# Kernel tuning notes

Hardware: AMD Instinct MI355X
Metric: run time of the kernel (lower is better)

Reference implementation:

```python
import jax, jax.numpy as jnp
import numpy as np

TEMPERATURE = 1.0
B, H, S, D = 2, 16, 2048, 128

def setup_inputs() -> dict:
    key = jax.random.key(0)
    kq, kk, kv = jax.random.split(key, 3)
    q = jax.random.normal(kq, (B, H, S, D), dtype=jnp.float32)
    k = jax.random.normal(kk, (B, H, S, D), dtype=jnp.float32)
    v = jax.random.normal(kv, (B, H, S, D), dtype=jnp.float32)
    alpha = jnp.float32(0.5)  # nn.Parameter(torch.tensor(0.5))
    return {"q": q, "k": k, "v": v, "alpha": alpha}

def reference(q, k, v, alpha):
    # scores: [B,H,S,S]
    scores = jnp.einsum('bhqd,bhkd->bhqk', q, k) / TEMPERATURE
    row_mean = jnp.mean(scores, axis=-1, keepdims=True)  # [B,H,S,1]
    adaptive = alpha * scores + (1.0 - alpha) * row_mean
    attn = jax.nn.softmax(adaptive, axis=-1)
    return jnp.einsum('bhqk,bhkd->bhqd', attn, v)
```

## Files before the change

### kernel.cpp

```cpp
#include <hip/hip_runtime.h>


#define S_LEN 2048
#define HD    128
#define BQ    64
#define BK    64
#define NW    2
#define NT    (S_LEN / BK)
#define KTILE_USH 8192
#define VTILE_USH 8192
#define VBASE_USH (32 * NT * KTILE_USH)

typedef __bf16    bf16x8 __attribute__((ext_vector_type(8)));
typedef __bf16    bf16x4 __attribute__((ext_vector_type(4)));
typedef _Float16  f16x8  __attribute__((ext_vector_type(8)));
typedef float     f32x4  __attribute__((ext_vector_type(4)));

__device__ __forceinline__ unsigned short f2bf(float x) {
  unsigned u = __builtin_bit_cast(unsigned, x);
  u = (u + 0x7FFFu + ((u >> 16) & 1u)) >> 16;
  return (unsigned short)u;
}
__device__ __forceinline__ unsigned short f2h(float x) {
  _Float16 h = (_Float16)x;
  return __builtin_bit_cast(unsigned short, h);
}
__device__ __forceinline__ float fast_exp2(float x) {
#if __has_builtin(__builtin_amdgcn_exp2f)
  return __builtin_amdgcn_exp2f(x);
#else
  return exp2f(x);
#endif
}

__global__ __launch_bounds__(256) void attn_prepass_kernel(
    const float* __restrict__ kg, const float* __restrict__ vg,
    unsigned short* __restrict__ ws) {
  __shared__ float T[64 * 130];
  const int blk  = blockIdx.x;
  const int head = blk >> 5;
  const int kt   = blk & 31;
  const int tid  = threadIdx.x;
  const size_t hoff = (size_t)head * S_LEN * HD;
  const float* kp = kg + hoff + (size_t)kt * BK * HD;
  const float* vp = vg + hoff + (size_t)kt * BK * HD;
  unsigned short* wsK = ws + (size_t)blk * KTILE_USH;
  unsigned short* wsV = ws + VBASE_USH + (size_t)blk * VTILE_USH;

#pragma unroll
  for (int it = 0; it < 4; ++it) {
    int idx = it * 256 + tid;
    int key = idx >> 4;
    int ch  = idx & 15;
    const float* src = kp + key * HD + ch * 8;
    float4 a = *(const float4*)src;
    float4 b = *(const float4*)(src + 4);
    float xs[8] = {a.x, a.y, a.z, a.w, b.x, b.y, b.z, b.w};
    union { unsigned short s[8]; uint4 v; } hi;
#pragma unroll
    for (int j = 0; j < 8; ++j) hi.s[j] = f2h(xs[j]);
    int slot = (ch & 8) | ((ch & 7) ^ (key & 7));
    *(uint4*)&wsK[key * 128 + slot * 8] = hi.v;
  }

#pragma unroll
  for (int it = 0; it < 16; ++it) {
    int idx = it * 256 + tid;
    int key = idx >> 6;
    int c2  = idx & 63;
    float2 a = *(const float2*)(vp + (size_t)key * HD + c2 * 2);
    *(float2*)&T[key * 130 + c2 * 2] = a;
  }
  __syncthreads();

#pragma unroll
  for (int r = 0; r < 4; ++r) {
    int idx = r * 256 + tid;
    int dim = idx >> 3;
    int ch  = idx & 7;
    union { unsigned short s[8]; uint4 v; } gg;
#pragma unroll
    for (int j = 0; j < 8; ++j) gg.s[j] = f2bf(T[(ch * 8 + j) * 130 + dim]);
    int gidx = ((dim >> 4) * 2 + (ch >> 2)) * 64 + (ch & 3) * 16 + (dim & 15);
    *(uint4*)&wsV[gidx * 8] = gg.v;
  }
}

__device__ __forceinline__ void stage_k(const unsigned short* __restrict__ wt,
                                        unsigned short* dst, int tid, int w) {
#pragma unroll
  for (int r = 0; r < 8; ++r) {
    const unsigned int* gp = (const unsigned int*)(wt + (size_t)(r * 128 + tid) * 8);
    unsigned short* lp = dst + (size_t)(r * 128 + w * 64) * 8;
    __builtin_amdgcn_global_load_lds(
        (const __attribute__((address_space(1))) unsigned int*)gp,
        (__attribute__((address_space(3))) unsigned int*)lp, 16, 0, 0);
  }
}

__global__ __launch_bounds__(128, 2) void adaptive_attn_kernel(
    const float* __restrict__ qg, const unsigned short* __restrict__ ws,
    const float* __restrict__ alphap, float* __restrict__ out) {
  __shared__ unsigned short sBuf[2][KTILE_USH];
  __shared__ unsigned short sP[NW][2][1024];

  const int b    = blockIdx.x;
  const int head = (b & 7) * 4 + ((b >> 3) & 3);
  const int qt   = b >> 5;

  const int tid  = threadIdx.x;
  const int w    = tid >> 6;
  const int lane = tid & 63;
  const int g    = lane >> 4;
  const int qi   = lane & 15;

  const float lscale = alphap[0] * 1.44269504088896f;

  f16x8 qf[2][4];
#pragma unroll
  for (int h = 0; h < 2; ++h) {
    const int qrow = qt * BQ + w * 32 + h * 16 + qi;
    const float* qp = qg + (size_t)head * S_LEN * HD + (size_t)qrow * HD;
#pragma unroll
    for (int c = 0; c < 4; ++c) {
      float4 a  = *(const float4*)(qp + c * 32 + g * 8);
      float4 bb = *(const float4*)(qp + c * 32 + g * 8 + 4);
      float xs[8] = {a.x, a.y, a.z, a.w, bb.x, bb.y, bb.z, bb.w};
      union { f16x8 v; _Float16 s[8]; } hh;
#pragma unroll
      for (int j = 0; j < 8; ++j) hh.s[j] = (_Float16)(xs[j] * lscale);
      qf[h][c] = hh.v;
    }
  }

  f32x4 o[2][8];
#pragma unroll
  for (int h = 0; h < 2; ++h)
#pragma unroll
    for (int dt = 0; dt < 8; ++dt) o[h][dt] = (f32x4){0.f, 0.f, 0.f, 0.f};
  float lrun[2] = {0.f, 0.f};

  const unsigned short* wsKh = ws + (size_t)head * NT * KTILE_USH;
  const unsigned short* wsVh = ws + VBASE_USH + (size_t)head * NT * VTILE_USH;

  stage_k(wsKh, &sBuf[0][0], tid, w);
  __syncthreads();

  for (int kt = 0; kt < NT; ++kt) {
    const unsigned short* sK = &sBuf[kt & 1][0];

    const unsigned short* vb = wsVh + (size_t)kt * VTILE_USH;
    bf16x8 vf[8][2];
#pragma unroll
    for (int dt = 0; dt < 8; ++dt)
#pragma unroll
      for (int c = 0; c < 2; ++c)
        vf[dt][c] = *(const bf16x8*)&vb[((dt * 2 + c) * 64 + lane) * 8];

    if (kt + 1 < NT)
      stage_k(wsKh + (size_t)(kt + 1) * KTILE_USH, &sBuf[(kt + 1) & 1][0], tid, w);

    f32x4 st[2][4];
    __builtin_amdgcn_s_setprio(1);
#pragma unroll
    for (int mt = 0; mt < 4; ++mt) {
      f32x4 a0 = (f32x4){0.f, 0.f, 0.f, 0.f};
      f32x4 a1 = (f32x4){0.f, 0.f, 0.f, 0.f};
#pragma unroll
      for (int c = 0; c < 4; ++c) {
        int ch   = c * 4 + g;
        int slot = (ch & 8) | ((ch & 7) ^ (qi & 7));
        f16x8 ah = *(const f16x8*)&sK[(mt * 16 + qi) * 128 + slot * 8];
        a0 = __builtin_amdgcn_mfma_f32_16x16x32_f16(ah, qf[0][c], a0, 0, 0, 0);
        a1 = __builtin_amdgcn_mfma_f32_16x16x32_f16(ah, qf[1][c], a1, 0, 0, 0);
      }
      st[0][mt] = a0; st[1][mt] = a1;
    }
    __builtin_amdgcn_s_setprio(0);

#pragma unroll
    for (int h = 0; h < 2; ++h) {
      unsigned short* sPh = &sP[w][h][0];
#pragma unroll
      for (int mt = 0; mt < 4; ++mt) {
        float p0 = fast_exp2(st[h][mt][0]);
        float p1 = fast_exp2(st[h][mt][1]);
        float p2 = fast_exp2(st[h][mt][2]);
        float p3 = fast_exp2(st[h][mt][3]);
        lrun[h] += (p0 + p1) + (p2 + p3);
        bf16x4 pv4;
        pv4[0] = (__bf16)p0; pv4[1] = (__bf16)p1;
        pv4[2] = (__bf16)p2; pv4[3] = (__bf16)p3;
        int slot = (mt * 2 + (g >> 1)) ^ (qi & 7);
        *(bf16x4*)&sPh[qi * 64 + slot * 8 + (g & 1) * 4] = pv4;
      }
    }

    bf16x8 pf[2][2];
#pragma unroll
    for (int h = 0; h < 2; ++h)
#pragma unroll
      for (int c = 0; c < 2; ++c) {
        int slot = (c * 4 + g) ^ (qi & 7);
        pf[h][c] = *(const bf16x8*)&sP[w][h][qi * 64 + slot * 8];
      }

    __builtin_amdgcn_s_setprio(1);
#pragma unroll
    for (int dt = 0; dt < 8; ++dt) {
      f32x4 a0 = o[0][dt];
      f32x4 a1 = o[1][dt];
#pragma unroll
      for (int c = 0; c < 2; ++c) {
        a0 = __builtin_amdgcn_mfma_f32_16x16x32_bf16(pf[0][c], vf[dt][c], a0, 0, 0, 0);
        a1 = __builtin_amdgcn_mfma_f32_16x16x32_bf16(pf[1][c], vf[dt][c], a1, 0, 0, 0);
      }
      o[0][dt] = a0; o[1][dt] = a1;
    }
    __builtin_amdgcn_s_setprio(0);

    __syncthreads();
  }

  float* oph = out + (size_t)head * S_LEN * HD + (size_t)(qt * BQ + w * 32) * HD;
#pragma unroll
  for (int h = 0; h < 2; ++h) {
    float ltot = lrun[h];
    ltot += __shfl_xor(ltot, 16, 64);
    ltot += __shfl_xor(ltot, 32, 64);
    float inv[4];
#pragma unroll
    for (int r = 0; r < 4; ++r) {
      float lr = __shfl(ltot, g * 4 + r, 64);
      inv[r] = 1.0f / lr;
    }
    float* op = oph + (size_t)(h * 16) * HD;
#pragma unroll
    for (int dt = 0; dt < 8; ++dt) {
#pragma unroll
      for (int r = 0; r < 4; ++r) {
        op[(size_t)(g * 4 + r) * HD + dt * 16 + qi] = o[h][dt][r] * inv[r];
      }
    }
  }
}

extern "C" void kernel_launch(void* const* d_in, const int* in_sizes, int n_in,
                              void* d_out, int out_size, void* d_ws, size_t ws_size,
                              hipStream_t stream) {
  const float* q     = (const float*)d_in[0];
  const float* k     = (const float*)d_in[1];
  const float* v     = (const float*)d_in[2];
  const float* alpha = (const float*)d_in[3];
  float* out = (float*)d_out;
  unsigned short* ws = (unsigned short*)d_ws;

  hipLaunchKernelGGL(attn_prepass_kernel, dim3(1024), dim3(256), 0, stream,
                     k, v, ws);
  hipLaunchKernelGGL(adaptive_attn_kernel, dim3(1024), dim3(128), 0, stream,
                     q, ws, alpha, out);
}
```

Baseline: 212.9 us.

## Interleave K and V into per-tile records and stage both through LDS

The prepass now writes K (fp16) and transposed V (bf16) for each 32-key tile into one contiguous 16KB record. The attention kernel stages the whole record into double-buffered LDS with global_load_lds and reads V fragments from LDS, where before it loaded them from global memory into registers. The key tile shrinks from 64 to 32, which doubles the loop iterations and barriers but lowers V register pressure. The s_setprio hints are also removed.

```diff
diff --git a/kernel.cpp b/kernel.cpp
--- a/kernel.cpp
+++ b/kernel.cpp
@@ -4,12 +4,9 @@
 #define S_LEN 2048
 #define HD    128
 #define BQ    64
-#define BK    64
-#define NW    2
+#define BK    32
 #define NT    (S_LEN / BK)
-#define KTILE_USH 8192
-#define VTILE_USH 8192
-#define VBASE_USH (32 * NT * KTILE_USH)
+#define REC_USH 8192
 
 typedef __bf16    bf16x8 __attribute__((ext_vector_type(8)));
 typedef __bf16    bf16x4 __attribute__((ext_vector_type(4)));
@@ -42,10 +39,10 @@
   const int kt   = blk & 31;
   const int tid  = threadIdx.x;
   const size_t hoff = (size_t)head * S_LEN * HD;
-  const float* kp = kg + hoff + (size_t)kt * BK * HD;
-  const float* vp = vg + hoff + (size_t)kt * BK * HD;
-  unsigned short* wsK = ws + (size_t)blk * KTILE_USH;
-  unsigned short* wsV = ws + VBASE_USH + (size_t)blk * VTILE_USH;
+  const float* kp = kg + hoff + (size_t)kt * 64 * HD;
+  const float* vp = vg + hoff + (size_t)kt * 64 * HD;
+  unsigned short* rec0 = ws + ((size_t)head * NT + kt * 2) * REC_USH;
+  unsigned short* rec1 = rec0 + REC_USH;
 
 #pragma unroll
   for (int it = 0; it < 4; ++it) {
@@ -60,7 +57,8 @@
 #pragma unroll
     for (int j = 0; j < 8; ++j) hi.s[j] = f2h(xs[j]);
     int slot = (ch & 8) | ((ch & 7) ^ (key & 7));
-    *(uint4*)&wsK[key * 128 + slot * 8] = hi.v;
+    unsigned short* wsK = (key < 32) ? rec0 : rec1;
+    *(uint4*)&wsK[(key & 31) * 128 + slot * 8] = hi.v;
   }
 
 #pragma unroll
@@ -81,13 +79,14 @@
     union { unsigned short s[8]; uint4 v; } gg;
 #pragma unroll
     for (int j = 0; j < 8; ++j) gg.s[j] = f2bf(T[(ch * 8 + j) * 130 + dim]);
-    int gidx = ((dim >> 4) * 2 + (ch >> 2)) * 64 + (ch & 3) * 16 + (dim & 15);
-    *(uint4*)&wsV[gidx * 8] = gg.v;
-  }
-}
-
-__device__ __forceinline__ void stage_k(const unsigned short* __restrict__ wt,
-                                        unsigned short* dst, int tid, int w) {
+    int slot = (ch & 3) ^ ((dim >> 1) & 3);
+    unsigned short* wsVt = ((ch < 4) ? rec0 : rec1) + 4096;
+    *(uint4*)&wsVt[dim * 32 + slot * 8] = gg.v;
+  }
+}
+
+__device__ __forceinline__ void stage_rec(const unsigned short* __restrict__ wt,
+                                          unsigned short* dst, int tid, int w) {
 #pragma unroll
   for (int r = 0; r < 8; ++r) {
     const unsigned int* gp = (const unsigned int*)(wt + (size_t)(r * 128 + tid) * 8);
@@ -101,8 +100,8 @@
 __global__ __launch_bounds__(128, 2) void adaptive_attn_kernel(
     const float* __restrict__ qg, const unsigned short* __restrict__ ws,
     const float* __restrict__ alphap, float* __restrict__ out) {
-  __shared__ unsigned short sBuf[2][KTILE_USH];
-  __shared__ unsigned short sP[NW][2][1024];
+  __shared__ unsigned short sBuf[2][REC_USH];
+  __shared__ unsigned short sP[2][2][1024];
 
   const int b    = blockIdx.x;
   const int head = (b & 7) * 4 + ((b >> 3) & 3);
@@ -140,30 +139,21 @@
     for (int dt = 0; dt < 8; ++dt) o[h][dt] = (f32x4){0.f, 0.f, 0.f, 0.f};
   float lrun[2] = {0.f, 0.f};
 
-  const unsigned short* wsKh = ws + (size_t)head * NT * KTILE_USH;
-  const unsigned short* wsVh = ws + VBASE_USH + (size_t)head * NT * VTILE_USH;
-
-  stage_k(wsKh, &sBuf[0][0], tid, w);
+  const unsigned short* wsh = ws + (size_t)head * NT * REC_USH;
+
+  stage_rec(wsh, &sBuf[0][0], tid, w);
   __syncthreads();
 
   for (int kt = 0; kt < NT; ++kt) {
-    const unsigned short* sK = &sBuf[kt & 1][0];
-
-    const unsigned short* vb = wsVh + (size_t)kt * VTILE_USH;
-    bf16x8 vf[8][2];
-#pragma unroll
-    for (int dt = 0; dt < 8; ++dt)
-#pragma unroll
-      for (int c = 0; c < 2; ++c)
-        vf[dt][c] = *(const bf16x8*)&vb[((dt * 2 + c) * 64 + lane) * 8];
+    const unsigned short* sK  = &sBuf[kt & 1][0];
+    const unsigned short* sVt = sK + 4096;
 
     if (kt + 1 < NT)
-      stage_k(wsKh + (size_t)(kt + 1) * KTILE_USH, &sBuf[(kt + 1) & 1][0], tid, w);
-
-    f32x4 st[2][4];
-    __builtin_amdgcn_s_setprio(1);
-#pragma unroll
-    for (int mt = 0; mt < 4; ++mt) {
+      stage_rec(wsh + (size_t)(kt + 1) * REC_USH, &sBuf[(kt + 1) & 1][0], tid, w);
+
+    f32x4 st[2][2];
+#pragma unroll
+    for (int mt = 0; mt < 2; ++mt) {
       f32x4 a0 = (f32x4){0.f, 0.f, 0.f, 0.f};
       f32x4 a1 = (f32x4){0.f, 0.f, 0.f, 0.f};
 #pragma unroll
@@ -176,13 +166,12 @@
       }
       st[0][mt] = a0; st[1][mt] = a1;
     }
-    __builtin_amdgcn_s_setprio(0);
 
 #pragma unroll
     for (int h = 0; h < 2; ++h) {
       unsigned short* sPh = &sP[w][h][0];
 #pragma unroll
-      for (int mt = 0; mt < 4; ++mt) {
+      for (int mt = 0; mt < 2; ++mt) {
         float p0 = fast_exp2(st[h][mt][0]);
         float p1 = fast_exp2(st[h][mt][1]);
         float p2 = fast_exp2(st[h][mt][2]);
@@ -196,28 +185,20 @@
       }
     }
 
-    bf16x8 pf[2][2];
-#pragma unroll
-    for (int h = 0; h < 2; ++h)
-#pragma unroll
-      for (int c = 0; c < 2; ++c) {
-        int slot = (c * 4 + g) ^ (qi & 7);
-        pf[h][c] = *(const bf16x8*)&sP[w][h][qi * 64 + slot * 8];
-      }
-
-    __builtin_amdgcn_s_setprio(1);
+    bf16x8 pf[2];
+#pragma unroll
+    for (int h = 0; h < 2; ++h) {
+      int slot = g ^ (qi & 7);
+      pf[h] = *(const bf16x8*)&sP[w][h][qi * 64 + slot * 8];
+    }
+
 #pragma unroll
     for (int dt = 0; dt < 8; ++dt) {
-      f32x4 a0 = o[0][dt];
-      f32x4 a1 = o[1][dt];
-#pragma unroll
-      for (int c = 0; c < 2; ++c) {
-        a0 = __builtin_amdgcn_mfma_f32_16x16x32_bf16(pf[0][c], vf[dt][c], a0, 0, 0, 0);
-        a1 = __builtin_amdgcn_mfma_f32_16x16x32_bf16(pf[1][c], vf[dt][c], a1, 0, 0, 0);
-      }
-      o[0][dt] = a0; o[1][dt] = a1;
-    }
-    __builtin_amdgcn_s_setprio(0);
+      int slot = g ^ ((qi >> 1) & 3);
+      bf16x8 vf = *(const bf16x8*)&sVt[(dt * 16 + qi) * 32 + slot * 8];
+      o[0][dt] = __builtin_amdgcn_mfma_f32_16x16x32_bf16(pf[0], vf, o[0][dt], 0, 0, 0);
+      o[1][dt] = __builtin_amdgcn_mfma_f32_16x16x32_bf16(pf[1], vf, o[1][dt], 0, 0, 0);
+    }
 
     __syncthreads();
   }
```

New measurement: 220.8 us. 1.04x slower.
